# Kernel tuning notes

Measured on AMD Instinct MI355X. Metric: run time of the kernel, lower is better.

## Reference

```python
import jax, jax.numpy as jnp
import numpy as np

D_IN, D_MODEL = 512, 256
B, N = 2, 512


def setup_inputs() -> dict:
    key = jax.random.key(0)
    ks = jax.random.split(key, 8)
    xav_x = float(np.sqrt(2.0 / (D_IN + D_MODEL)))
    xav_p = float(np.sqrt(2.0 / (4 + D_MODEL)))
    return {
        "x": jax.random.normal(ks[0], (B, N, D_IN), dtype=jnp.float32),
        "pos": jax.random.normal(ks[1], (B, N, 4), dtype=jnp.float32),
        "attn_mask": jax.random.randint(ks[2], (B, N, N), 0, 2, dtype=jnp.int32),
        "Wx": jax.random.normal(ks[3], (D_IN, D_MODEL), dtype=jnp.float32) * xav_x,
        "bx": jnp.zeros((D_MODEL,), dtype=jnp.float32),
        "Wp": jax.random.normal(ks[4], (4, D_MODEL), dtype=jnp.float32) * xav_p,
        "bp": jnp.zeros((D_MODEL,), dtype=jnp.float32),
        "w": jax.random.normal(ks[5], (D_MODEL,), dtype=jnp.float32) * 0.05,
    }


def reference(x, pos, attn_mask, Wx, bx, Wp, bp, w):
    # projected, activated inputs: [B, N, d_model]
    h = jnp.tanh(x @ Wx + bx)
    # pairwise relative positions: [B, N, N, 4]
    rel = pos[:, :, None, :] - pos[:, None, :, :]
    # position MLP + tanh: [B, N, N, d_model]
    z = jnp.tanh(rel @ Wp + bp)
    # scores via dot with weight vector: [B, N, N]
    attn = jnp.einsum("bijd,d->bij", z, w)
    mask = attn_mask != 0
    attn = jnp.where(mask, attn, -jnp.inf)
    attn = jax.nn.softmax(attn, axis=2)
    attn = jnp.where(mask, attn, 0.0)
    # dropout is identity in eval mode
    # weighted sum: [B, N, d_model]
    output = jnp.einsum("bij,bjd->bid", attn, h)
    return (output, attn)
```

## Files before the change

### kernel.cpp

```cpp
#include <hip/hip_runtime.h>
#include <hip/hip_bf16.h>
#include <math.h>

#define BATCH   2
#define SEQ     512
#define DIN     512
#define DM      256

#define LOG2E2  2.88539008177792681f

#if __has_builtin(__builtin_amdgcn_exp2f)
#define EXP2(x) __builtin_amdgcn_exp2f(x)
#else
#define EXP2(x) exp2f(x)
#endif
#if __has_builtin(__builtin_amdgcn_rcpf)
#define RCP(x) __builtin_amdgcn_rcpf(x)
#else
#define RCP(x) (1.0f / (x))
#endif

__device__ __forceinline__ float tanh_from_scaled(float targ) {
    return fmaf(-2.0f, RCP(1.0f + EXP2(targ)), 1.0f);
}

__global__ __launch_bounds__(512) void prep_k(
    const float* __restrict__ pos,
    const float* __restrict__ Wp,
    const float* __restrict__ bp,
    const float* __restrict__ x,
    const float* __restrict__ Wx,
    const float* __restrict__ bx,
    float* __restrict__ EA,
    float2* __restrict__ EB2,
    float* __restrict__ h)
{
    const int tid = threadIdx.x;

    if (blockIdx.x < 256) {
        const int b  = blockIdx.x >> 7;
        const int tg = blockIdx.x & 127;
        const int d0 = 2 * tg, d1 = d0 + 1;

        const float4 p = ((const float4*)pos)[b * SEQ + tid];
        const float P0 = fmaf(p.x, Wp[d0], fmaf(p.y, Wp[DM + d0],
                         fmaf(p.z, Wp[2*DM + d0], p.w * Wp[3*DM + d0])));
        const float P1 = fmaf(p.x, Wp[d1], fmaf(p.y, Wp[DM + d1],
                         fmaf(p.z, Wp[2*DM + d1], p.w * Wp[3*DM + d1])));
        EB2[((size_t)(b * 128 + tg)) * SEQ + tid] =
            make_float2(EXP2(-LOG2E2 * P0), EXP2(-LOG2E2 * P1));
        return;
    }

    __shared__ float4 s_x[2][DIN/4];
    __shared__ float4 s_part[2][7][64];

    const int row0 = (blockIdx.x - 256) * 2;

    {
        const int r2  = __builtin_amdgcn_readfirstlane(tid >> 8);
        const int d   = tid & 255;
        const int row = row0 + r2;
        const float4 p = ((const float4*)pos)[row];
        const float P = fmaf(p.x, Wp[d],
                        fmaf(p.y, Wp[DM + d],
                        fmaf(p.z, Wp[2*DM + d],
                             p.w * Wp[3*DM + d])));
        EA[(size_t)row * DM + d] = EXP2(LOG2E2 * (P + bp[d]));
    }

    if (tid < 256) {
        const int r   = tid >> 7;
        const int idx = tid & 127;
        s_x[r][idx] = ((const float4*)(x + (size_t)(row0 + r) * DIN))[idx];
    }
    __syncthreads();

    const int w = tid >> 6;
    const int l = tid & 63;

    float4 acc0 = make_float4(0.f, 0.f, 0.f, 0.f);
    float4 acc1 = make_float4(0.f, 0.f, 0.f, 0.f);
    const float* __restrict__ wxp = Wx + 4 * l;

    #pragma unroll 2
    for (int k4 = 0; k4 < 16; k4++) {
        const int kk = w * 16 + k4;
        const float4 xv0 = s_x[0][kk];
        const float4 xv1 = s_x[1][kk];
        const float4 w0 = *(const float4*)(wxp + (size_t)(4*kk + 0) * DM);
        const float4 w1 = *(const float4*)(wxp + (size_t)(4*kk + 1) * DM);
        const float4 w2 = *(const float4*)(wxp + (size_t)(4*kk + 2) * DM);
        const float4 w3 = *(const float4*)(wxp + (size_t)(4*kk + 3) * DM);
        acc0.x = fmaf(xv0.x, w0.x, acc0.x); acc0.y = fmaf(xv0.x, w0.y, acc0.y);
        acc0.z = fmaf(xv0.x, w0.z, acc0.z); acc0.w = fmaf(xv0.x, w0.w, acc0.w);
        acc0.x = fmaf(xv0.y, w1.x, acc0.x); acc0.y = fmaf(xv0.y, w1.y, acc0.y);
        acc0.z = fmaf(xv0.y, w1.z, acc0.z); acc0.w = fmaf(xv0.y, w1.w, acc0.w);
        acc0.x = fmaf(xv0.z, w2.x, acc0.x); acc0.y = fmaf(xv0.z, w2.y, acc0.y);
        acc0.z = fmaf(xv0.z, w2.z, acc0.z); acc0.w = fmaf(xv0.z, w2.w, acc0.w);
        acc0.x = fmaf(xv0.w, w3.x, acc0.x); acc0.y = fmaf(xv0.w, w3.y, acc0.y);
        acc0.z = fmaf(xv0.w, w3.z, acc0.z); acc0.w = fmaf(xv0.w, w3.w, acc0.w);
        acc1.x = fmaf(xv1.x, w0.x, acc1.x); acc1.y = fmaf(xv1.x, w0.y, acc1.y);
        acc1.z = fmaf(xv1.x, w0.z, acc1.z); acc1.w = fmaf(xv1.x, w0.w, acc1.w);
        acc1.x = fmaf(xv1.y, w1.x, acc1.x); acc1.y = fmaf(xv1.y, w1.y, acc1.y);
        acc1.z = fmaf(xv1.y, w1.z, acc1.z); acc1.w = fmaf(xv1.y, w1.w, acc1.w);
        acc1.x = fmaf(xv1.z, w2.x, acc1.x); acc1.y = fmaf(xv1.z, w2.y, acc1.y);
        acc1.z = fmaf(xv1.z, w2.z, acc1.z); acc1.w = fmaf(xv1.z, w2.w, acc1.w);
        acc1.x = fmaf(xv1.w, w3.x, acc1.x); acc1.y = fmaf(xv1.w, w3.y, acc1.y);
        acc1.z = fmaf(xv1.w, w3.z, acc1.z); acc1.w = fmaf(xv1.w, w3.w, acc1.w);
    }

    if (w) {
        s_part[0][w - 1][l] = acc0;
        s_part[1][w - 1][l] = acc1;
    }
    __syncthreads();
    if (w == 0) {
        const float4 b4 = ((const float4*)bx)[l];
        acc0.x += b4.x; acc0.y += b4.y; acc0.z += b4.z; acc0.w += b4.w;
        acc1.x += b4.x; acc1.y += b4.y; acc1.z += b4.z; acc1.w += b4.w;
        #pragma unroll
        for (int q = 0; q < 7; q++) {
            const float4 q0 = s_part[0][q][l];
            const float4 q1 = s_part[1][q][l];
            acc0.x += q0.x; acc0.y += q0.y; acc0.z += q0.z; acc0.w += q0.w;
            acc1.x += q1.x; acc1.y += q1.y; acc1.z += q1.z; acc1.w += q1.w;
        }
        float4 t0, t1;
        t0.x = tanh_from_scaled(LOG2E2 * acc0.x);
        t0.y = tanh_from_scaled(LOG2E2 * acc0.y);
        t0.z = tanh_from_scaled(LOG2E2 * acc0.z);
        t0.w = tanh_from_scaled(LOG2E2 * acc0.w);
        t1.x = tanh_from_scaled(LOG2E2 * acc1.x);
        t1.y = tanh_from_scaled(LOG2E2 * acc1.y);
        t1.z = tanh_from_scaled(LOG2E2 * acc1.z);
        t1.w = tanh_from_scaled(LOG2E2 * acc1.w);
        ((float4*)(h + (size_t)row0 * DM))[l]       = t0;
        ((float4*)(h + (size_t)(row0 + 1) * DM))[l] = t1;
    }
}

__global__ __launch_bounds__(1024) void attn_k(
    const int*   __restrict__ mask,
    const float* __restrict__ wv,
    const float* __restrict__ EA,
    const float2* __restrict__ EB2,
    const float* __restrict__ h,
    float* __restrict__ out,
    float* __restrict__ attn_out)
{
    const int b   = blockIdx.x >> 7;
    const int i0  = (blockIdx.x & 127) * 4;
    const int tid = threadIdx.x;
    const int l   = tid & 63;
    const int j   = tid & 511;
    const int rg  = __builtin_amdgcn_readfirstlane(tid >> 9);

    __shared__ float4 s_ea[128][2];
    __shared__ float  s_o[3][4][DM];
    __shared__ float  s_red[4][8];

    if (tid < 256) {
        const int t = tid >> 1;
        const int g = tid & 1;
        const float2 ea_a = *(const float2*)(EA + (size_t)(b * SEQ + i0 + 2*g) * DM + 2*t);
        const float2 ea_b = *(const float2*)(EA + (size_t)(b * SEQ + i0 + 2*g + 1) * DM + 2*t);
        s_ea[t][g] = make_float4(ea_a.x, ea_a.y, ea_b.x, ea_b.y);
    }
    __syncthreads();

    const float2* __restrict__ EBj = EB2 + (size_t)b * 128 * SEQ + j;
    const float4* __restrict__ eap = &s_ea[0][rg];

    float aA = 0.f, aB = 0.f;
    #pragma unroll 8
    for (int t = 0; t < 128; t++) {
        const float2 eb = EBj[(size_t)t * SEQ];
        const float4 q  = eap[2 * t];
        const float  w0 = wv[2*t];
        const float  w1 = wv[2*t + 1];
        const float yA0 = fmaf(q.x, eb.x, 1.0f);
        const float yA1 = fmaf(q.y, eb.y, 1.0f);
        const float yB0 = fmaf(q.z, eb.x, 1.0f);
        const float yB1 = fmaf(q.w, eb.y, 1.0f);
        aA = fmaf(fmaf(w1, yA0, w0 * yA1), RCP(yA0 * yA1), aA);
        aB = fmaf(fmaf(w1, yB0, w0 * yB1), RCP(yB0 * yB1), aB);
    }

    const size_t mrowA = (size_t)b * SEQ * SEQ + (size_t)(i0 + 2*rg) * SEQ + j;
    const int mA = mask[mrowA];
    const int mB = mask[mrowA + SEQ];

    float pA = mA ? EXP2(-LOG2E2 * aA) : 0.f;
    float pB = mB ? EXP2(-LOG2E2 * aB) : 0.f;

    float sA = pA, sB = pB;
    #pragma unroll
    for (int off = 32; off; off >>= 1) {
        sA += __shfl_xor(sA, off, 64);
        sB += __shfl_xor(sB, off, 64);
    }
    const int w = tid >> 6;
    if (l == 0) {
        s_red[2*rg][w & 7]     = sA;
        s_red[2*rg + 1][w & 7] = sB;
    }
    __syncthreads();

    const float4 ra = ((const float4*)s_red[2*rg])[0],     rb = ((const float4*)s_red[2*rg])[1];
    const float4 rc = ((const float4*)s_red[2*rg + 1])[0], rd = ((const float4*)s_red[2*rg + 1])[1];
    pA *= __fdividef(1.0f, (ra.x+ra.y+ra.z+ra.w) + (rb.x+rb.y+rb.z+rb.w));
    pB *= __fdividef(1.0f, (rc.x+rc.y+rc.z+rc.w) + (rd.x+rd.y+rd.z+rd.w));

    attn_out[mrowA]       = pA;
    attn_out[mrowA + SEQ] = pB;
    __syncthreads();

    const int jq = __builtin_amdgcn_readfirstlane(tid >> 8);
    const int d  = tid & 255;
    const float* __restrict__ hp  = h + (size_t)(b * SEQ + jq * 128) * DM + d;
    const float* __restrict__ ar0 = attn_out + (size_t)b * SEQ * SEQ
                                  + (size_t)i0 * SEQ + jq * 128;
    const float* __restrict__ ar1 = ar0 + SEQ;
    const float* __restrict__ ar2 = ar0 + 2*SEQ;
    const float* __restrict__ ar3 = ar0 + 3*SEQ;

    float c0 = 0.f, c1 = 0.f, c2 = 0.f, c3 = 0.f;
    #pragma unroll 2
    for (int q = 0; q < 32; q++) {
        const float4 P0 = *(const float4*)(ar0 + 4*q);
        const float4 P1 = *(const float4*)(ar1 + 4*q);
        const float4 P2 = *(const float4*)(ar2 + 4*q);
        const float4 P3 = *(const float4*)(ar3 + 4*q);
        const float h0 = hp[(size_t)(4*q + 0) * DM];
        const float h1 = hp[(size_t)(4*q + 1) * DM];
        const float h2 = hp[(size_t)(4*q + 2) * DM];
        const float h3 = hp[(size_t)(4*q + 3) * DM];
        c0 = fmaf(P0.x, h0, fmaf(P0.y, h1, fmaf(P0.z, h2, fmaf(P0.w, h3, c0))));
        c1 = fmaf(P1.x, h0, fmaf(P1.y, h1, fmaf(P1.z, h2, fmaf(P1.w, h3, c1))));
        c2 = fmaf(P2.x, h0, fmaf(P2.y, h1, fmaf(P2.z, h2, fmaf(P2.w, h3, c2))));
        c3 = fmaf(P3.x, h0, fmaf(P3.y, h1, fmaf(P3.z, h2, fmaf(P3.w, h3, c3))));
    }

    if (jq > 0) {
        s_o[jq - 1][0][d] = c0;
        s_o[jq - 1][1][d] = c1;
        s_o[jq - 1][2][d] = c2;
        s_o[jq - 1][3][d] = c3;
    }
    __syncthreads();
    if (jq == 0) {
        float* __restrict__ op = out + (size_t)(b * SEQ + i0) * DM + d;
        op[0]    = c0 + s_o[0][0][d] + s_o[1][0][d] + s_o[2][0][d];
        op[DM]   = c1 + s_o[0][1][d] + s_o[1][1][d] + s_o[2][1][d];
        op[2*DM] = c2 + s_o[0][2][d] + s_o[1][2][d] + s_o[2][2][d];
        op[3*DM] = c3 + s_o[0][3][d] + s_o[1][3][d] + s_o[2][3][d];
    }
}

extern "C" void kernel_launch(void* const* d_in, const int* in_sizes, int n_in,
                              void* d_out, int out_size, void* d_ws, size_t ws_size,
                              hipStream_t stream) {
    const float* x    = (const float*)d_in[0];
    const float* pos  = (const float*)d_in[1];
    const int*   mask = (const int*)  d_in[2];
    const float* Wx   = (const float*)d_in[3];
    const float* bx   = (const float*)d_in[4];
    const float* Wp   = (const float*)d_in[5];
    const float* bp   = (const float*)d_in[6];
    const float* wv   = (const float*)d_in[7];

    float* out      = (float*)d_out;
    float* attn_out = (float*)d_out + (size_t)BATCH*SEQ*DM;

    char*   ws  = (char*)d_ws;
    float*  h   = (float*)(ws);
    float*  EA  = (float*)(ws + (size_t)BATCH*SEQ*DM*4);
    float2* EB2 = (float2*)(ws + 2*(size_t)BATCH*SEQ*DM*4);

    prep_k<<<256 + (BATCH*SEQ)/2, 512, 0, stream>>>(pos, Wp, bp, x, Wx, bx, EA, EB2, h);
    attn_k<<<(BATCH*SEQ)/4, 1024, 0, stream>>>(mask, wv, EA, EB2, h, out, attn_out);
}
```

Measured before the change: 119.6 us.

## Split score reduction over t across thread halves with two rows per block

Each block now handles 2 query rows instead of 4, and the grid doubles to 512 blocks. The two 512-thread halves each sum half of the 128 position-feature pairs for the same rows and combine their partial scores through shared memory. This doubles the block count for better CU occupancy and halves each thread's serial loop. In exchange, every EB2 column is read twice as often across blocks, there is an extra barrier, and the second half sits idle during softmax.

Result: no change. 120.9 us (+1.1%).

```diff
diff --git a/kernel.cpp b/kernel.cpp
--- a/kernel.cpp
+++ b/kernel.cpp
@@ -149,34 +149,33 @@
     float* __restrict__ out,
     float* __restrict__ attn_out)
 {
-    const int b   = blockIdx.x >> 7;
-    const int i0  = (blockIdx.x & 127) * 4;
+    const int b   = blockIdx.x >> 8;
+    const int i0  = (blockIdx.x & 255) * 2;
     const int tid = threadIdx.x;
     const int l   = tid & 63;
     const int j   = tid & 511;
-    const int rg  = __builtin_amdgcn_readfirstlane(tid >> 9);
-
-    __shared__ float4 s_ea[128][2];
-    __shared__ float  s_o[3][4][DM];
-    __shared__ float  s_red[4][8];
-
-    if (tid < 256) {
-        const int t = tid >> 1;
-        const int g = tid & 1;
-        const float2 ea_a = *(const float2*)(EA + (size_t)(b * SEQ + i0 + 2*g) * DM + 2*t);
-        const float2 ea_b = *(const float2*)(EA + (size_t)(b * SEQ + i0 + 2*g + 1) * DM + 2*t);
-        s_ea[t][g] = make_float4(ea_a.x, ea_a.y, ea_b.x, ea_b.y);
+    const int th  = __builtin_amdgcn_readfirstlane(tid >> 9);
+
+    __shared__ float4 s_ea[128];
+    __shared__ float  s_ap[2][SEQ];
+    __shared__ float  s_o[3][2][DM];
+    __shared__ float  s_red[2][8];
+
+    if (tid < 128) {
+        const float2 ea_a = *(const float2*)(EA + (size_t)(b * SEQ + i0) * DM + 2*tid);
+        const float2 ea_b = *(const float2*)(EA + (size_t)(b * SEQ + i0 + 1) * DM + 2*tid);
+        s_ea[tid] = make_float4(ea_a.x, ea_a.y, ea_b.x, ea_b.y);
     }
     __syncthreads();
 
     const float2* __restrict__ EBj = EB2 + (size_t)b * 128 * SEQ + j;
-    const float4* __restrict__ eap = &s_ea[0][rg];
+    const int t0 = th * 64;
 
     float aA = 0.f, aB = 0.f;
     #pragma unroll 8
-    for (int t = 0; t < 128; t++) {
+    for (int t = t0; t < t0 + 64; t++) {
         const float2 eb = EBj[(size_t)t * SEQ];
-        const float4 q  = eap[2 * t];
+        const float4 q  = s_ea[t];
         const float  w0 = wv[2*t];
         const float  w1 = wv[2*t + 1];
         const float yA0 = fmaf(q.x, eb.x, 1.0f);
@@ -187,33 +186,44 @@
         aB = fmaf(fmaf(w1, yB0, w0 * yB1), RCP(yB0 * yB1), aB);
     }
 
-    const size_t mrowA = (size_t)b * SEQ * SEQ + (size_t)(i0 + 2*rg) * SEQ + j;
-    const int mA = mask[mrowA];
-    const int mB = mask[mrowA + SEQ];
-
-    float pA = mA ? EXP2(-LOG2E2 * aA) : 0.f;
-    float pB = mB ? EXP2(-LOG2E2 * aB) : 0.f;
-
-    float sA = pA, sB = pB;
-    #pragma unroll
-    for (int off = 32; off; off >>= 1) {
-        sA += __shfl_xor(sA, off, 64);
-        sB += __shfl_xor(sB, off, 64);
-    }
-    const int w = tid >> 6;
-    if (l == 0) {
-        s_red[2*rg][w & 7]     = sA;
-        s_red[2*rg + 1][w & 7] = sB;
-    }
-    __syncthreads();
-
-    const float4 ra = ((const float4*)s_red[2*rg])[0],     rb = ((const float4*)s_red[2*rg])[1];
-    const float4 rc = ((const float4*)s_red[2*rg + 1])[0], rd = ((const float4*)s_red[2*rg + 1])[1];
-    pA *= __fdividef(1.0f, (ra.x+ra.y+ra.z+ra.w) + (rb.x+rb.y+rb.z+rb.w));
-    pB *= __fdividef(1.0f, (rc.x+rc.y+rc.z+rc.w) + (rd.x+rd.y+rd.z+rd.w));
-
-    attn_out[mrowA]       = pA;
-    attn_out[mrowA + SEQ] = pB;
+    if (th == 1) {
+        s_ap[0][j] = aA;
+        s_ap[1][j] = aB;
+    }
+    __syncthreads();
+
+    const size_t mrowA = (size_t)b * SEQ * SEQ + (size_t)i0 * SEQ + j;
+    float pA = 0.f, pB = 0.f;
+    if (th == 0) {
+        aA += s_ap[0][j];
+        aB += s_ap[1][j];
+        const int mA = mask[mrowA];
+        const int mB = mask[mrowA + SEQ];
+        pA = mA ? EXP2(-LOG2E2 * aA) : 0.f;
+        pB = mB ? EXP2(-LOG2E2 * aB) : 0.f;
+
+        float sA = pA, sB = pB;
+        #pragma unroll
+        for (int off = 32; off; off >>= 1) {
+            sA += __shfl_xor(sA, off, 64);
+            sB += __shfl_xor(sB, off, 64);
+        }
+        if (l == 0) {
+            const int wj = tid >> 6;
+            s_red[0][wj] = sA;
+            s_red[1][wj] = sB;
+        }
+    }
+    __syncthreads();
+
+    if (th == 0) {
+        const float4 ra = ((const float4*)s_red[0])[0], rb = ((const float4*)s_red[0])[1];
+        const float4 rc = ((const float4*)s_red[1])[0], rd = ((const float4*)s_red[1])[1];
+        pA *= __fdividef(1.0f, (ra.x+ra.y+ra.z+ra.w) + (rb.x+rb.y+rb.z+rb.w));
+        pB *= __fdividef(1.0f, (rc.x+rc.y+rc.z+rc.w) + (rd.x+rd.y+rd.z+rd.w));
+        attn_out[mrowA]       = pA;
+        attn_out[mrowA + SEQ] = pB;
+    }
     __syncthreads();
 
     const int jq = __builtin_amdgcn_readfirstlane(tid >> 8);
@@ -222,39 +232,29 @@
     const float* __restrict__ ar0 = attn_out + (size_t)b * SEQ * SEQ
                                   + (size_t)i0 * SEQ + jq * 128;
     const float* __restrict__ ar1 = ar0 + SEQ;
-    const float* __restrict__ ar2 = ar0 + 2*SEQ;
-    const float* __restrict__ ar3 = ar0 + 3*SEQ;
-
-    float c0 = 0.f, c1 = 0.f, c2 = 0.f, c3 = 0.f;
-    #pragma unroll 2
+
+    float c0 = 0.f, c1 = 0.f;
+    #pragma unroll 4
     for (int q = 0; q < 32; q++) {
         const float4 P0 = *(const float4*)(ar0 + 4*q);
         const float4 P1 = *(const float4*)(ar1 + 4*q);
-        const float4 P2 = *(const float4*)(ar2 + 4*q);
-        const float4 P3 = *(const float4*)(ar3 + 4*q);
         const float h0 = hp[(size_t)(4*q + 0) * DM];
         const float h1 = hp[(size_t)(4*q + 1) * DM];
         const float h2 = hp[(size_t)(4*q + 2) * DM];
         const float h3 = hp[(size_t)(4*q + 3) * DM];
         c0 = fmaf(P0.x, h0, fmaf(P0.y, h1, fmaf(P0.z, h2, fmaf(P0.w, h3, c0))));
         c1 = fmaf(P1.x, h0, fmaf(P1.y, h1, fmaf(P1.z, h2, fmaf(P1.w, h3, c1))));
-        c2 = fmaf(P2.x, h0, fmaf(P2.y, h1, fmaf(P2.z, h2, fmaf(P2.w, h3, c2))));
-        c3 = fmaf(P3.x, h0, fmaf(P3.y, h1, fmaf(P3.z, h2, fmaf(P3.w, h3, c3))));
     }
 
     if (jq > 0) {
         s_o[jq - 1][0][d] = c0;
         s_o[jq - 1][1][d] = c1;
-        s_o[jq - 1][2][d] = c2;
-        s_o[jq - 1][3][d] = c3;
     }
     __syncthreads();
     if (jq == 0) {
         float* __restrict__ op = out + (size_t)(b * SEQ + i0) * DM + d;
-        op[0]    = c0 + s_o[0][0][d] + s_o[1][0][d] + s_o[2][0][d];
-        op[DM]   = c1 + s_o[0][1][d] + s_o[1][1][d] + s_o[2][1][d];
-        op[2*DM] = c2 + s_o[0][2][d] + s_o[1][2][d] + s_o[2][2][d];
-        op[3*DM] = c3 + s_o[0][3][d] + s_o[1][3][d] + s_o[2][3][d];
+        op[0]  = c0 + s_o[0][0][d] + s_o[1][0][d] + s_o[2][0][d];
+        op[DM] = c1 + s_o[0][1][d] + s_o[1][1][d] + s_o[2][1][d];
     }
 }
 
@@ -279,5 +279,5 @@
     float2* EB2 = (float2*)(ws + 2*(size_t)BATCH*SEQ*DM*4);
 
     prep_k<<<256 + (BATCH*SEQ)/2, 512, 0, stream>>>(pos, Wp, bp, x, Wx, bx, EA, EB2, h);
-    attn_k<<<(BATCH*SEQ)/4, 1024, 0, stream>>>(mask, wv, EA, EB2, h, out, attn_out);
-}
+    attn_k<<<(BATCH*SEQ)/2, 1024, 0, stream>>>(mask, wv, EA, EB2, h, out, attn_out);
+}
```
